# Kernel tuning notes

Hardware: AMD Instinct MI355X
Metric: run time of the kernel (lower is better)

## Reference

```python
import math
import jax, jax.numpy as jnp
import numpy as np

NLAT, NLON = 61, 120
C, H = 64, 4
DH = C // H
HID = 128
NSEG = NLAT * NLON  # number of grid points / softmax segments
EPS = 1e-6
SCALE = 1.0 / math.sqrt(DH)


def _build_geometry():
    """Neighbor pairs within theta_cutoff on the equiangular (pole-including) grid.

    The neighborhood structure is longitude-shift invariant, so we enumerate it
    for output longitude 0 and replicate with a modular longitude shift.
    """
    nlat, nlon = NLAT, NLON
    theta = np.pi * np.arange(nlat) / (nlat - 1)           # colatitudes incl. poles
    lam = 2.0 * np.pi * np.arange(nlon) / nlon
    theta_cutoff = 7.0 / math.sqrt(math.pi) * math.pi / (nlat - 1)
    ct, st = np.cos(theta), np.sin(theta)
    # great-circle distance between (theta_o, 0) and (theta_i, dlon): [nlat, nlat, nlon]
    cosd = (ct[:, None, None] * ct[None, :, None]
            + st[:, None, None] * st[None, :, None] * np.cos(lam)[None, None, :])
    dist = np.arccos(np.clip(cosd, -1.0, 1.0))
    ho, hi, dl = np.nonzero(dist <= theta_cutoff)          # E reference-column entries
    wo = np.arange(nlon)
    out_idx = (ho[:, None] * nlon + wo[None, :]).reshape(-1).astype(np.int32)
    in_idx = (hi[:, None] * nlon + (dl[:, None] + wo[None, :]) % nlon).reshape(-1).astype(np.int32)
    # quadrature (integration) weights: sin(theta) measure, zero at the poles
    w = (st * (np.pi / (nlat - 1)) * (2.0 * np.pi / nlon)).astype(np.float32)
    quad_w = np.repeat(w, nlon)                            # [NSEG]
    return jnp.asarray(out_idx), jnp.asarray(in_idx), jnp.asarray(quad_w)


def setup_inputs() -> dict:
    key = jax.random.key(0)
    ks = jax.random.split(key, 8)
    out_idx, in_idx, quad_w = _build_geometry()

    def w(k, shape, fan_in):
        return jax.random.normal(k, shape, dtype=jnp.float32) / np.float32(np.sqrt(fan_in))

    return {
        "x": jax.random.normal(ks[0], (1, C, NLAT, NLON), dtype=jnp.float32),
        "wq": w(ks[1], (C, C), C),
        "wk": w(ks[2], (C, C), C),
        "wv": w(ks[3], (C, C), C),
        "wo": w(ks[4], (C, C), C),
        "w1": w(ks[5], (HID, C), C),
        "b1": jnp.zeros((HID,), jnp.float32),
        "w2": w(ks[6], (C, HID), HID),
        "b2": jnp.zeros((C,), jnp.float32),
        "ln0_g": jnp.ones((C,), jnp.float32),
        "ln0_b": jnp.zeros((C,), jnp.float32),
        "ln1_g": jnp.ones((C,), jnp.float32),
        "ln1_b": jnp.zeros((C,), jnp.float32),
        "quad_w": quad_w,
        "out_idx": out_idx,
        "in_idx": in_idx,
    }


def _layernorm(x, g, b):
    # channel-wise LayerNorm at every spatial location; x: [B, C, H, W]
    m = jnp.mean(x, axis=1, keepdims=True)
    v = jnp.mean((x - m) ** 2, axis=1, keepdims=True)
    xh = (x - m) * jax.lax.rsqrt(v + EPS)
    return xh * g[None, :, None, None] + b[None, :, None, None]


def _neighborhood_attn(x, wq, wk, wv, wo, quad_w, out_idx, in_idx):
    # x: [B, C, nlat, nlon] (fp32)
    B = x.shape[0]
    q = jnp.einsum('oc,bchw->bohw', wq, x).reshape(B, H, DH, NSEG)
    k = jnp.einsum('oc,bchw->bohw', wk, x).reshape(B, H, DH, NSEG)
    v = jnp.einsum('oc,bchw->bohw', wv, x).reshape(B, H, DH, NSEG)
    qg = q[..., out_idx]                                   # [B,H,DH,NNZ]
    kg = k[..., in_idx]
    s = jnp.einsum('bhdn,bhdn->bhn', qg, kg) * SCALE       # [B,H,NNZ]
    s = jnp.moveaxis(s, -1, 0)                             # [NNZ,B,H]
    smax = jax.ops.segment_max(s, out_idx, num_segments=NSEG)
    # quadrature-weighted, numerically stable softmax over each neighborhood
    alpha = jnp.exp(s - smax[out_idx]) * quad_w[in_idx][:, None, None]
    vg = jnp.moveaxis(v[..., in_idx], -1, 0)               # [NNZ,B,H,DH]
    num = jax.ops.segment_sum(alpha[..., None] * vg, out_idx, num_segments=NSEG)
    den = jax.ops.segment_sum(alpha, out_idx, num_segments=NSEG)
    att = num / den[..., None]                             # [NSEG,B,H,DH]
    att = jnp.moveaxis(att, 0, -1).reshape(B, C, NLAT, NLON)
    return jnp.einsum('oc,bchw->bohw', wo, att)


def reference(x, wq, wk, wv, wo, w1, b1, w2, b2, ln0_g, ln0_b, ln1_g, ln1_b,
              quad_w, out_idx, in_idx):
    residual = x
    h0 = _layernorm(x, ln0_g, ln0_b)
    a = _neighborhood_attn(h0.astype(jnp.float32), wq, wk, wv, wo,
                           quad_w, out_idx, in_idx).astype(x.dtype)
    x1 = a + residual
    h1 = _layernorm(x1, ln1_g, ln1_b)
    m = jax.nn.gelu(jnp.einsum('fc,bchw->bfhw', w1, h1) + b1[None, :, None, None],
                    approximate=False)
    m = jnp.einsum('cf,bfhw->bchw', w2, m) + b2[None, :, None, None]
    return m + x1
```

## Files before the change

kernel.cpp:

```cpp
#include <hip/hip_runtime.h>
#include <math.h>

#define NSEG 7320
#define NLON 120
#define HIDN 128

__global__ __launch_bounds__(256) void k0_meta(const int* __restrict__ out_idx,
                                               const int* __restrict__ in_idx,
                                               const float* __restrict__ qw,
                                               int E, int* __restrict__ row_start,
                                               int4* __restrict__ meta)
{
    int e = blockIdx.x * 256 + threadIdx.x;
    if (e >= E) return;
    int ho = out_idx[e * NLON] / NLON;
    if (e == 0) {
        row_start[ho] = 0;
    } else {
        int hp = out_idx[(e - 1) * NLON] / NLON;
        if (hp != ho) row_start[ho] = e;
    }
    if (e == E - 1) row_start[ho + 1] = E;

    int i0 = in_idx[e * NLON];
    int hi = i0 / NLON;
    int dl = i0 - hi * NLON;
    meta[e] = make_int4(hi * NLON, dl, __float_as_int(qw[i0]), 0);
}

__global__ __launch_bounds__(64) void k1_ln_qkv(
    const float* __restrict__ x,  const float* __restrict__ wq,
    const float* __restrict__ wk, const float* __restrict__ wv,
    const float* __restrict__ g,  const float* __restrict__ b,
    float* __restrict__ q_nm, float* __restrict__ k_nm,
    float* __restrict__ v_nm, float* __restrict__ x_nm)
{
    __shared__ __align__(16) float sm[64 * 20];
    const int lane = threadIdx.x;
    const int tile = blockIdx.x;
    const int grp  = blockIdx.y;
    const int n    = tile * 64 + lane;
    const bool act = n < NSEG;
    const int nn   = act ? n : (NSEG - 1);

    float xv[64];
    float s = 0.f, s2 = 0.f;
#pragma unroll
    for (int c = 0; c < 64; ++c) { float t = x[c * NSEG + nn]; xv[c] = t; s += t; s2 += t * t; }

    if (grp == 12) {
        for (int ob = 0; ob < 64; ob += 16) {
#pragma unroll
            for (int j = 0; j < 16; ++j) sm[lane * 20 + j] = xv[ob + j];
            __builtin_amdgcn_wave_barrier();
#pragma unroll
            for (int it = 0; it < 4; ++it) {
                int i  = it * 16 + (lane >> 2);
                int j4 = (lane & 3) * 4;
                int np = tile * 64 + i;
                if (np < NSEG)
                    *(float4*)&x_nm[(size_t)np * 64 + ob + j4] = *(const float4*)&sm[i * 20 + j4];
            }
            __builtin_amdgcn_wave_barrier();
        }
        return;
    }

    float mean = s * 0.015625f;
    float var  = s2 * 0.015625f - mean * mean;
    float rstd = rsqrtf(var + 1e-6f);
#pragma unroll
    for (int c = 0; c < 64; ++c) xv[c] = (xv[c] - mean) * rstd * g[c] + b[c];

    const int mm    = grp >> 2;
    const int obase = (grp & 3) * 16;
    const float* __restrict__ w = (mm == 0) ? wq : (mm == 1) ? wk : wv;
    float* __restrict__ dst = (mm == 0) ? q_nm : (mm == 1) ? k_nm : v_nm;
    const float scale = (mm == 0) ? 0.25f : 1.0f;

#pragma unroll
    for (int j = 0; j < 16; ++j) {
        int o = obase + j;
        float acc = 0.f;
#pragma unroll
        for (int c = 0; c < 64; ++c) acc += w[o * 64 + c] * xv[c];
        sm[lane * 20 + j] = acc * scale;
    }
    __builtin_amdgcn_wave_barrier();
#pragma unroll
    for (int it = 0; it < 4; ++it) {
        int i  = it * 16 + (lane >> 2);
        int j4 = (lane & 3) * 4;
        int np = tile * 64 + i;
        if (np < NSEG)
            *(float4*)&dst[(size_t)np * 64 + obase + j4] = *(const float4*)&sm[i * 20 + j4];
    }
}

__global__ __launch_bounds__(256) void k2_attn(
    const float* __restrict__ q_nm, const float* __restrict__ k_nm,
    const float* __restrict__ v_nm, const float* __restrict__ x_nm,
    const float* __restrict__ wo,
    const int4* __restrict__ meta,  const int* __restrict__ row_start,
    float* __restrict__ x1_pl, float* __restrict__ out)
{
    __shared__ __align__(16) float smq[4][64];
    __shared__ __align__(16) float sma[4][64][4];
    __shared__ unsigned            smo[4][64];
    __shared__ __align__(16) float smatt[4][64];
    __shared__ float               smx1[64][5];

    const int tid  = threadIdx.x;
    const int wv   = tid >> 6;
    const int lane = tid & 63;
    const int seg  = blockIdx.x * 4 + wv;
    const int ho   = seg / NLON;
    const int wlon = seg - ho * NLON;
    const int e0   = row_start[ho];
    const int e1   = row_start[ho + 1];

    smq[wv][lane] = q_nm[(size_t)seg * 64 + lane];
    __builtin_amdgcn_wave_barrier();

    const int g    = lane >> 4;
    const int qd   = lane & 15;
    const int head = qd >> 2;

    float d0 = 0.f, d1 = 0.f, d2 = 0.f, d3 = 0.f;
    float4 num = make_float4(0.f, 0.f, 0.f, 0.f);

    for (int eb = e0; eb < e1; eb += 64) {
        int rem = e1 - eb; if (rem > 64) rem = 64;
        const bool actl = lane < rem;
        int e = eb + (actl ? lane : 0);
        int4 mt = meta[e];
        int dlw = mt.y + wlon; if (dlw >= NLON) dlw -= NLON;
        int in  = mt.x + dlw;
        float qwv = actl ? __int_as_float(mt.z) : 0.f;

        const float* __restrict__ kr = k_nm + (size_t)in * 64;
        float s0 = 0.f, s1 = 0.f, s2 = 0.f, s3 = 0.f;
#pragma unroll
        for (int c4 = 0; c4 < 16; ++c4) {
            float4 kv = *(const float4*)(kr + c4 * 4);
            float4 qv = *(const float4*)&smq[wv][c4 * 4];
            float dd = kv.x * qv.x + kv.y * qv.y + kv.z * qv.z + kv.w * qv.w;
            if      (c4 < 4)  s0 += dd;
            else if (c4 < 8)  s1 += dd;
            else if (c4 < 12) s2 += dd;
            else              s3 += dd;
        }
        float a0 = __expf(s0) * qwv;
        float a1 = __expf(s1) * qwv;
        float a2 = __expf(s2) * qwv;
        float a3 = __expf(s3) * qwv;
        d0 += a0; d1 += a1; d2 += a2; d3 += a3;

        *(float4*)&sma[wv][lane][0] = make_float4(a0, a1, a2, a3);
        smo[wv][lane] = (unsigned)in << 8;
        __builtin_amdgcn_wave_barrier();

        int nj = (rem + 3) >> 2;
        for (int jj = 0; jj < nj; ++jj) {
            int j = jj * 4 + g;
            float al     = sma[wv][j][head];
            unsigned off = smo[wv][j];
            float4 vv = *(const float4*)((const char*)v_nm + off + qd * 16);
            num.x += al * vv.x; num.y += al * vv.y;
            num.z += al * vv.z; num.w += al * vv.w;
        }
        __builtin_amdgcn_wave_barrier();
    }

    num.x += __shfl_xor(num.x, 16); num.y += __shfl_xor(num.y, 16);
    num.z += __shfl_xor(num.z, 16); num.w += __shfl_xor(num.w, 16);
    num.x += __shfl_xor(num.x, 32); num.y += __shfl_xor(num.y, 32);
    num.z += __shfl_xor(num.z, 32); num.w += __shfl_xor(num.w, 32);
#pragma unroll
    for (int off = 1; off < 64; off <<= 1) {
        d0 += __shfl_xor(d0, off); d1 += __shfl_xor(d1, off);
        d2 += __shfl_xor(d2, off); d3 += __shfl_xor(d3, off);
    }
    float dh = (head == 0) ? d0 : (head == 1) ? d1 : (head == 2) ? d2 : d3;
    float rd = 1.0f / dh;
    if (lane < 16) {
        float4 att = make_float4(num.x * rd, num.y * rd, num.z * rd, num.w * rd);
        *(float4*)&smatt[wv][lane * 4] = att;
    }
    __builtin_amdgcn_wave_barrier();

    const float4* __restrict__ wr = (const float4*)(wo + lane * 64);
    float acc = 0.f;
#pragma unroll
    for (int c4 = 0; c4 < 16; ++c4) {
        float4 w4 = wr[c4];
        acc += w4.x * smatt[wv][c4 * 4 + 0] + w4.y * smatt[wv][c4 * 4 + 1]
             + w4.z * smatt[wv][c4 * 4 + 2] + w4.w * smatt[wv][c4 * 4 + 3];
    }
    float x1v = acc + x_nm[(size_t)seg * 64 + lane];

    smx1[lane][wv] = x1v;
    __syncthreads();
    int c  = tid >> 2;
    int sl = tid & 3;
    float ov = smx1[c][sl];
    int seg0 = blockIdx.x * 4;
    out[c * NSEG + seg0 + sl]   = ov;
    x1_pl[c * NSEG + seg0 + sl] = ov;
}

__global__ __launch_bounds__(64) void k3_mlp(
    const float* __restrict__ x1, const float* __restrict__ w1,
    const float* __restrict__ b1, const float* __restrict__ w2,
    const float* __restrict__ b2, const float* __restrict__ g,
    const float* __restrict__ bb, float* __restrict__ out)
{
    const int lane = threadIdx.x;
    const int tile = blockIdx.x;
    const int grp  = blockIdx.y;
    const int n    = tile * 64 + lane;
    const bool act = n < NSEG;
    const int nn   = act ? n : (NSEG - 1);

    float xv[64];
    float s = 0.f, s2 = 0.f;
#pragma unroll
    for (int c = 0; c < 64; ++c) { float t = x1[c * NSEG + nn]; xv[c] = t; s += t; s2 += t * t; }
    float mean = s * 0.015625f;
    float var  = s2 * 0.015625f - mean * mean;
    float rstd = rsqrtf(var + 1e-6f);
#pragma unroll
    for (int c = 0; c < 64; ++c) xv[c] = (xv[c] - mean) * rstd * g[c] + bb[c];

    const int h0 = grp * 16;
    float gh[16];
#pragma unroll
    for (int j = 0; j < 16; ++j) {
        int h = h0 + j;
        float mh = b1[h];
#pragma unroll
        for (int c = 0; c < 64; ++c) mh += w1[h * 64 + c] * xv[c];
        gh[j] = 0.5f * mh * (1.0f + erff(mh * 0.70710678118654752f));
    }

    if (act) {
#pragma unroll
        for (int c = 0; c < 64; ++c) {
            float acc = (grp == 0) ? b2[c] : 0.f;
#pragma unroll
            for (int j = 0; j < 16; ++j) acc += w2[c * HIDN + h0 + j] * gh[j];
            atomicAdd(&out[c * NSEG + n], acc);
        }
    }
}

extern "C" void kernel_launch(void* const* d_in, const int* in_sizes, int n_in,
                              void* d_out, int out_size, void* d_ws, size_t ws_size,
                              hipStream_t stream)
{
    const float* x    = (const float*)d_in[0];
    const float* wq   = (const float*)d_in[1];
    const float* wk   = (const float*)d_in[2];
    const float* wv   = (const float*)d_in[3];
    const float* wo   = (const float*)d_in[4];
    const float* w1   = (const float*)d_in[5];
    const float* b1   = (const float*)d_in[6];
    const float* w2   = (const float*)d_in[7];
    const float* b2   = (const float*)d_in[8];
    const float* ln0g = (const float*)d_in[9];
    const float* ln0b = (const float*)d_in[10];
    const float* ln1g = (const float*)d_in[11];
    const float* ln1b = (const float*)d_in[12];
    const float* qw   = (const float*)d_in[13];
    const int* out_idx = (const int*)d_in[14];
    const int* in_idx  = (const int*)d_in[15];
    float* out = (float*)d_out;

    const int NNZ = in_sizes[15];
    const int E   = NNZ / NLON;
    const size_t N64 = (size_t)NSEG * 64;

    float* ws   = (float*)d_ws;
    float* q_nm = ws;
    float* k_nm = ws + N64;
    float* v_nm = ws + 2 * N64;
    float* x_nm = ws + 3 * N64;
    float* x1   = ws + 4 * N64;
    int* row_start = (int*)(ws + 5 * N64);
    int4* meta = (int4*)(ws + 5 * N64 + 64);

    hipLaunchKernelGGL(k0_meta, dim3((E + 255) / 256), dim3(256), 0, stream,
                       out_idx, in_idx, qw, E, row_start, meta);
    hipLaunchKernelGGL(k1_ln_qkv, dim3(115, 13), dim3(64), 0, stream,
                       x, wq, wk, wv, ln0g, ln0b, q_nm, k_nm, v_nm, x_nm);
    hipLaunchKernelGGL(k2_attn, dim3(1830), dim3(256), 0, stream,
                       q_nm, k_nm, v_nm, x_nm, wo, meta, row_start, x1, out);
    hipLaunchKernelGGL(k3_mlp, dim3(115, 8), dim3(64), 0, stream,
                       x1, w1, b1, w2, b2, ln1g, ln1b, out);
}
```

Before: 224.6 us.

## Fold metadata into QKV kernel, simplify attention loop, split MLP without atomics

The separate metadata kernel is merged into the QKV launch as extra grid rows, which removes one launch. The attention kernel drops its shared-memory batched scheme for a per-edge loop where each lane holds one channel and reduces the dot product over a head with shuffles. Blocks are interleaved from both ends of the grid to balance work across latitude rows. The MLP is split into two kernels that pass GELU activations through a workspace buffer, replacing atomicAdd accumulation and the out-initialisation store. The cost is a serial per-edge dependency chain in attention and extra global traffic for the activations.

```diff
diff --git a/kernel.cpp b/kernel.cpp
--- a/kernel.cpp
+++ b/kernel.cpp
@@ -4,44 +4,43 @@
 #define NSEG 7320
 #define NLON 120
 #define HIDN 128
-
-__global__ __launch_bounds__(256) void k0_meta(const int* __restrict__ out_idx,
-                                               const int* __restrict__ in_idx,
-                                               const float* __restrict__ qw,
-                                               int E, int* __restrict__ row_start,
-                                               int4* __restrict__ meta)
-{
-    int e = blockIdx.x * 256 + threadIdx.x;
-    if (e >= E) return;
-    int ho = out_idx[e * NLON] / NLON;
-    if (e == 0) {
-        row_start[ho] = 0;
-    } else {
-        int hp = out_idx[(e - 1) * NLON] / NLON;
-        if (hp != ho) row_start[ho] = e;
-    }
-    if (e == E - 1) row_start[ho + 1] = E;
-
-    int i0 = in_idx[e * NLON];
-    int hi = i0 / NLON;
-    int dl = i0 - hi * NLON;
-    meta[e] = make_int4(hi * NLON, dl, __float_as_int(qw[i0]), 0);
-}
 
 __global__ __launch_bounds__(64) void k1_ln_qkv(
     const float* __restrict__ x,  const float* __restrict__ wq,
     const float* __restrict__ wk, const float* __restrict__ wv,
     const float* __restrict__ g,  const float* __restrict__ b,
+    const int* __restrict__ out_idx, const int* __restrict__ in_idx,
+    const float* __restrict__ qw, int E,
     float* __restrict__ q_nm, float* __restrict__ k_nm,
-    float* __restrict__ v_nm, float* __restrict__ x_nm)
+    float* __restrict__ v_nm, float* __restrict__ x_nm,
+    int* __restrict__ row_start, int4* __restrict__ meta)
 {
     __shared__ __align__(16) float sm[64 * 20];
     const int lane = threadIdx.x;
     const int tile = blockIdx.x;
     const int grp  = blockIdx.y;
-    const int n    = tile * 64 + lane;
+
+    if (grp >= 13) {
+        int e = ((grp - 13) * 115 + tile) * 64 + lane;
+        if (e >= E) return;
+        int ho = out_idx[e * NLON] / NLON;
+        if (e == 0) {
+            row_start[ho] = 0;
+        } else {
+            int hp = out_idx[(e - 1) * NLON] / NLON;
+            if (hp != ho) row_start[ho] = e;
+        }
+        if (e == E - 1) row_start[ho + 1] = E;
+        int i0 = in_idx[e * NLON];
+        int hi = i0 / NLON;
+        int dl = i0 - hi * NLON;
+        meta[e] = make_int4(hi * NLON, dl, __float_as_int(qw[i0]), 0);
+        return;
+    }
+
+    const int n   = tile * 64 + lane;
     const bool act = n < NSEG;
-    const int nn   = act ? n : (NSEG - 1);
+    const int nn  = act ? n : (NSEG - 1);
 
     float xv[64];
     float s = 0.f, s2 = 0.f;
@@ -102,91 +101,44 @@
     const float* __restrict__ v_nm, const float* __restrict__ x_nm,
     const float* __restrict__ wo,
     const int4* __restrict__ meta,  const int* __restrict__ row_start,
-    float* __restrict__ x1_pl, float* __restrict__ out)
-{
-    __shared__ __align__(16) float smq[4][64];
-    __shared__ __align__(16) float sma[4][64][4];
-    __shared__ unsigned            smo[4][64];
+    float* __restrict__ x1_pl)
+{
     __shared__ __align__(16) float smatt[4][64];
-    __shared__ float               smx1[64][5];
+    __shared__ float smx1[64][5];
 
     const int tid  = threadIdx.x;
     const int wv   = tid >> 6;
     const int lane = tid & 63;
-    const int seg  = blockIdx.x * 4 + wv;
+
+    const int bu   = blockIdx.x >> 1;
+    const int seg0 = (blockIdx.x & 1) ? (NSEG - 4 - bu * 4) : (bu * 4);
+    const int seg  = seg0 + wv;
     const int ho   = seg / NLON;
-    const int wlon = seg - ho * NLON;
-    const int e0   = row_start[ho];
-    const int e1   = row_start[ho + 1];
-
-    smq[wv][lane] = q_nm[(size_t)seg * 64 + lane];
-    __builtin_amdgcn_wave_barrier();
-
-    const int g    = lane >> 4;
-    const int qd   = lane & 15;
-    const int head = qd >> 2;
-
-    float d0 = 0.f, d1 = 0.f, d2 = 0.f, d3 = 0.f;
-    float4 num = make_float4(0.f, 0.f, 0.f, 0.f);
-
-    for (int eb = e0; eb < e1; eb += 64) {
-        int rem = e1 - eb; if (rem > 64) rem = 64;
-        const bool actl = lane < rem;
-        int e = eb + (actl ? lane : 0);
+    const int wlon = __builtin_amdgcn_readfirstlane(seg - ho * NLON);
+    int e0 = __builtin_amdgcn_readfirstlane(row_start[ho]);
+    int e1 = __builtin_amdgcn_readfirstlane(row_start[ho + 1]);
+
+    const float qreg = q_nm[(size_t)seg * 64 + lane];
+    float num = 0.f, den = 0.f;
+
+#pragma unroll 2
+    for (int e = e0; e < e1; ++e) {
         int4 mt = meta[e];
         int dlw = mt.y + wlon; if (dlw >= NLON) dlw -= NLON;
         int in  = mt.x + dlw;
-        float qwv = actl ? __int_as_float(mt.z) : 0.f;
-
-        const float* __restrict__ kr = k_nm + (size_t)in * 64;
-        float s0 = 0.f, s1 = 0.f, s2 = 0.f, s3 = 0.f;
-#pragma unroll
-        for (int c4 = 0; c4 < 16; ++c4) {
-            float4 kv = *(const float4*)(kr + c4 * 4);
-            float4 qv = *(const float4*)&smq[wv][c4 * 4];
-            float dd = kv.x * qv.x + kv.y * qv.y + kv.z * qv.z + kv.w * qv.w;
-            if      (c4 < 4)  s0 += dd;
-            else if (c4 < 8)  s1 += dd;
-            else if (c4 < 12) s2 += dd;
-            else              s3 += dd;
-        }
-        float a0 = __expf(s0) * qwv;
-        float a1 = __expf(s1) * qwv;
-        float a2 = __expf(s2) * qwv;
-        float a3 = __expf(s3) * qwv;
-        d0 += a0; d1 += a1; d2 += a2; d3 += a3;
-
-        *(float4*)&sma[wv][lane][0] = make_float4(a0, a1, a2, a3);
-        smo[wv][lane] = (unsigned)in << 8;
-        __builtin_amdgcn_wave_barrier();
-
-        int nj = (rem + 3) >> 2;
-        for (int jj = 0; jj < nj; ++jj) {
-            int j = jj * 4 + g;
-            float al     = sma[wv][j][head];
-            unsigned off = smo[wv][j];
-            float4 vv = *(const float4*)((const char*)v_nm + off + qd * 16);
-            num.x += al * vv.x; num.y += al * vv.y;
-            num.z += al * vv.z; num.w += al * vv.w;
-        }
-        __builtin_amdgcn_wave_barrier();
-    }
-
-    num.x += __shfl_xor(num.x, 16); num.y += __shfl_xor(num.y, 16);
-    num.z += __shfl_xor(num.z, 16); num.w += __shfl_xor(num.w, 16);
-    num.x += __shfl_xor(num.x, 32); num.y += __shfl_xor(num.y, 32);
-    num.z += __shfl_xor(num.z, 32); num.w += __shfl_xor(num.w, 32);
-#pragma unroll
-    for (int off = 1; off < 64; off <<= 1) {
-        d0 += __shfl_xor(d0, off); d1 += __shfl_xor(d1, off);
-        d2 += __shfl_xor(d2, off); d3 += __shfl_xor(d3, off);
-    }
-    float dh = (head == 0) ? d0 : (head == 1) ? d1 : (head == 2) ? d2 : d3;
-    float rd = 1.0f / dh;
-    if (lane < 16) {
-        float4 att = make_float4(num.x * rd, num.y * rd, num.z * rd, num.w * rd);
-        *(float4*)&smatt[wv][lane * 4] = att;
-    }
+        float kd = k_nm[(size_t)in * 64 + lane];
+        float vd = v_nm[(size_t)in * 64 + lane];
+        float p  = kd * qreg;
+        p += __shfl_xor(p, 1);
+        p += __shfl_xor(p, 2);
+        p += __shfl_xor(p, 4);
+        p += __shfl_xor(p, 8);
+        float a = __expf(p) * __int_as_float(mt.z);
+        num = fmaf(a, vd, num);
+        den += a;
+    }
+
+    smatt[wv][lane] = num / den;
     __builtin_amdgcn_wave_barrier();
 
     const float4* __restrict__ wr = (const float4*)(wo + lane * 64);
@@ -203,22 +155,16 @@
     __syncthreads();
     int c  = tid >> 2;
     int sl = tid & 3;
-    float ov = smx1[c][sl];
-    int seg0 = blockIdx.x * 4;
-    out[c * NSEG + seg0 + sl]   = ov;
-    x1_pl[c * NSEG + seg0 + sl] = ov;
-}
-
-__global__ __launch_bounds__(64) void k3_mlp(
+    x1_pl[c * NSEG + seg0 + sl] = smx1[c][sl];
+}
+
+__global__ __launch_bounds__(64) void k3a_mlp1(
     const float* __restrict__ x1, const float* __restrict__ w1,
-    const float* __restrict__ b1, const float* __restrict__ w2,
-    const float* __restrict__ b2, const float* __restrict__ g,
-    const float* __restrict__ bb, float* __restrict__ out)
+    const float* __restrict__ b1, const float* __restrict__ g,
+    const float* __restrict__ bb, float* __restrict__ m_act)
 {
     const int lane = threadIdx.x;
-    const int tile = blockIdx.x;
-    const int grp  = blockIdx.y;
-    const int n    = tile * 64 + lane;
+    const int n    = blockIdx.x * 64 + lane;
     const bool act = n < NSEG;
     const int nn   = act ? n : (NSEG - 1);
 
@@ -232,25 +178,41 @@
 #pragma unroll
     for (int c = 0; c < 64; ++c) xv[c] = (xv[c] - mean) * rstd * g[c] + bb[c];
 
-    const int h0 = grp * 16;
-    float gh[16];
-#pragma unroll
-    for (int j = 0; j < 16; ++j) {
+    const int h0 = blockIdx.y * 32;
+    if (!act) return;
+#pragma unroll
+    for (int j = 0; j < 32; ++j) {
         int h = h0 + j;
         float mh = b1[h];
 #pragma unroll
         for (int c = 0; c < 64; ++c) mh += w1[h * 64 + c] * xv[c];
-        gh[j] = 0.5f * mh * (1.0f + erff(mh * 0.70710678118654752f));
-    }
-
-    if (act) {
-#pragma unroll
-        for (int c = 0; c < 64; ++c) {
-            float acc = (grp == 0) ? b2[c] : 0.f;
-#pragma unroll
-            for (int j = 0; j < 16; ++j) acc += w2[c * HIDN + h0 + j] * gh[j];
-            atomicAdd(&out[c * NSEG + n], acc);
-        }
+        m_act[h * NSEG + n] = 0.5f * mh * (1.0f + erff(mh * 0.70710678118654752f));
+    }
+}
+
+__global__ __launch_bounds__(64) void k3b_mlp2(
+    const float* __restrict__ m_act, const float* __restrict__ w2,
+    const float* __restrict__ b2,    const float* __restrict__ x1,
+    float* __restrict__ out)
+{
+    const int lane = threadIdx.x;
+    const int n    = blockIdx.x * 64 + lane;
+    if (n >= NSEG) return;
+    const int c0   = blockIdx.y * 16;
+
+    float acc[16];
+#pragma unroll
+    for (int j = 0; j < 16; ++j) acc[j] = 0.f;
+
+    for (int h = 0; h < HIDN; ++h) {
+        float mh = m_act[h * NSEG + n];
+#pragma unroll
+        for (int j = 0; j < 16; ++j) acc[j] += w2[(c0 + j) * HIDN + h] * mh;
+    }
+#pragma unroll
+    for (int j = 0; j < 16; ++j) {
+        int c = c0 + j;
+        out[c * NSEG + n] = acc[j] + b2[c] + x1[c * NSEG + n];
     }
 }
 
@@ -280,21 +242,23 @@
     const int E   = NNZ / NLON;
     const size_t N64 = (size_t)NSEG * 64;
 
-    float* ws   = (float*)d_ws;
-    float* q_nm = ws;
-    float* k_nm = ws + N64;
-    float* v_nm = ws + 2 * N64;
-    float* x_nm = ws + 3 * N64;
-    float* x1   = ws + 4 * N64;
-    int* row_start = (int*)(ws + 5 * N64);
-    int4* meta = (int4*)(ws + 5 * N64 + 64);
-
-    hipLaunchKernelGGL(k0_meta, dim3((E + 255) / 256), dim3(256), 0, stream,
-                       out_idx, in_idx, qw, E, row_start, meta);
-    hipLaunchKernelGGL(k1_ln_qkv, dim3(115, 13), dim3(64), 0, stream,
-                       x, wq, wk, wv, ln0g, ln0b, q_nm, k_nm, v_nm, x_nm);
+    float* ws    = (float*)d_ws;
+    float* q_nm  = ws;
+    float* k_nm  = ws + N64;
+    float* v_nm  = ws + 2 * N64;
+    float* x_nm  = ws + 3 * N64;
+    float* x1    = ws + 4 * N64;
+    float* m_act = ws + 5 * N64;
+    int* row_start = (int*)(ws + 7 * N64);
+    int4* meta = (int4*)(ws + 7 * N64 + 64);
+
+    hipLaunchKernelGGL(k1_ln_qkv, dim3(115, 15), dim3(64), 0, stream,
+                       x, wq, wk, wv, ln0g, ln0b, out_idx, in_idx, qw, E,
+                       q_nm, k_nm, v_nm, x_nm, row_start, meta);
     hipLaunchKernelGGL(k2_attn, dim3(1830), dim3(256), 0, stream,
-                       q_nm, k_nm, v_nm, x_nm, wo, meta, row_start, x1, out);
-    hipLaunchKernelGGL(k3_mlp, dim3(115, 8), dim3(64), 0, stream,
-                       x1, w1, b1, w2, b2, ln1g, ln1b, out);
-}
+                       q_nm, k_nm, v_nm, x_nm, wo, meta, row_start, x1);
+    hipLaunchKernelGGL(k3a_mlp1, dim3(115, 4), dim3(64), 0, stream,
+                       x1, w1, b1, ln1g, ln1b, m_act);
+    hipLaunchKernelGGL(k3b_mlp2, dim3(115, 4), dim3(64), 0, stream,
+                       m_act, w2, b2, x1, out);
+}
```

Result: slower. 352.2 us (+56.8%).
